# Kernel optimization log

Measured on AMD Instinct MI355X. Metric: run time of the kernel, lower is better.

Reference implementation:

```python
import jax, jax.numpy as jnp
import numpy as np

N, C, H, W = 64, 384, 56, 56   # local feature map
M, D = 16, 384                  # global tokens, d_model


def setup_inputs() -> dict:
    key = jax.random.key(0)
    k0, k1, k2, k3 = jax.random.split(key, 4)
    local_feature = jax.random.normal(k0, (N, C, H, W), dtype=jnp.float32)
    x = jax.random.normal(k1, (N, M, D), dtype=jnp.float32)
    # nn.Linear params: weight [out, in], bias [out]
    Wq = jax.random.normal(k2, (C, D), dtype=jnp.float32) * (1.0 / np.sqrt(D))
    bq = jnp.zeros((C,), dtype=jnp.float32)
    Wu = jax.random.normal(k3, (D, C), dtype=jnp.float32) * (1.0 / np.sqrt(C))
    bu = jnp.zeros((D,), dtype=jnp.float32)
    return {"local_feature": local_feature, "x": x, "Wq": Wq, "bq": bq, "Wu": Wu, "bu": bu}


def reference(local_feature, x, Wq, bq, Wu, bu):
    n, c, h, w = local_feature.shape
    # n c h w -> n (h w) c
    lf = local_feature.reshape(n, c, h * w).transpose(0, 2, 1)  # [n, L, c]
    q = x @ Wq.T + bq                                           # [n, M, c]
    scores = jnp.einsum('nmc,nlc->nml', q, lf) * (c ** -0.5)    # [n, M, L]
    attn = jax.nn.softmax(scores, axis=-1)
    fusion = jnp.einsum('nml,nlc->nmc', attn, lf)               # [n, M, c]
    return fusion @ Wu.T + bu + x                               # residual to x
```

## Files before the change

kernel.cpp:

```cpp
#include <hip/hip_runtime.h>
#include <math.h>

#define N_ 64
#define C_ 384
#define L_ 3136
#define M_ 16
#define D_ 384

__global__ __launch_bounds__(128) void k1_qproj(const float* __restrict__ x,
                                                const float* __restrict__ Wq,
                                                const float* __restrict__ bq,
                                                float* __restrict__ qs) {
    const int n = blockIdx.x;
    const int c = blockIdx.y * 128 + threadIdx.x;
    const float4* __restrict__ wrow = (const float4*)(Wq + (size_t)c * D_);
    const float4* __restrict__ xn   = (const float4*)(x + (size_t)n * M_ * D_);
    float acc[M_];
#pragma unroll
    for (int m = 0; m < M_; ++m) acc[m] = 0.f;
    for (int dq = 0; dq < D_ / 4; ++dq) {
        const float4 wv = wrow[dq];
#pragma unroll
        for (int m = 0; m < M_; ++m) {
            const float4 xv = xn[m * (D_ / 4) + dq];
            acc[m] += wv.x * xv.x + wv.y * xv.y + wv.z * xv.z + wv.w * xv.w;
        }
    }
    const float rs = 0.05103103630798287f;
    const float b = bq[c];
    float* qout = qs + ((size_t)n * C_ + c) * M_;
#pragma unroll
    for (int m = 0; m < M_; ++m) qout[m] = (acc[m] + b) * rs;
}

__global__ __launch_bounds__(256) void k2_scores(const float* __restrict__ lf,
                                                 const float* __restrict__ qs,
                                                 float* __restrict__ scores) {
    const int n = blockIdx.x;
    const int s = blockIdx.y;
    const int t = threadIdx.x;
    const bool active = (t < 224);
    const int l0 = s * 448 + (active ? t : 0) * 2;
    const float* __restrict__ lfn = lf + (size_t)n * C_ * L_;
    const float* __restrict__ qn  = qs + (size_t)n * C_ * M_;
    float accx[M_], accy[M_];
#pragma unroll
    for (int m = 0; m < M_; ++m) { accx[m] = 0.f; accy[m] = 0.f; }
    if (active) {
#pragma unroll 4
        for (int c = 0; c < C_; ++c) {
            const float2 lv = *(const float2*)(lfn + (size_t)c * L_ + l0);
            const float* __restrict__ qv = qn + c * M_;
#pragma unroll
            for (int m = 0; m < M_; ++m) {
                accx[m] += qv[m] * lv.x;
                accy[m] += qv[m] * lv.y;
            }
        }
        float* sn = scores + (size_t)n * M_ * L_;
#pragma unroll
        for (int m = 0; m < M_; ++m) {
            *(float2*)(sn + (size_t)m * L_ + l0) = make_float2(accx[m], accy[m]);
        }
    }
}

__global__ __launch_bounds__(64) void k3_softmax(float* __restrict__ scores) {
    float* row = scores + (size_t)blockIdx.x * L_;
    const int t = threadIdx.x;
    float lmax = -1e30f;
    for (int i = t; i < L_ / 4; i += 64) {
        const float4 v = ((const float4*)row)[i];
        lmax = fmaxf(lmax, fmaxf(fmaxf(v.x, v.y), fmaxf(v.z, v.w)));
    }
#pragma unroll
    for (int o = 32; o > 0; o >>= 1) lmax = fmaxf(lmax, __shfl_xor(lmax, o, 64));
    float lsum = 0.f;
    for (int i = t; i < L_ / 4; i += 64) {
        const float4 v = ((const float4*)row)[i];
        lsum += expf(v.x - lmax) + expf(v.y - lmax) +
                expf(v.z - lmax) + expf(v.w - lmax);
    }
#pragma unroll
    for (int o = 32; o > 0; o >>= 1) lsum += __shfl_xor(lsum, o, 64);
    const float inv = 1.0f / lsum;
    for (int i = t; i < L_ / 4; i += 64) {
        float4 v = ((const float4*)row)[i];
        v.x = expf(v.x - lmax) * inv;
        v.y = expf(v.y - lmax) * inv;
        v.z = expf(v.z - lmax) * inv;
        v.w = expf(v.w - lmax) * inv;
        ((float4*)row)[i] = v;
    }
}

__global__ __launch_bounds__(384) void k4_fusion(const float* __restrict__ lf,
                                                 const float* __restrict__ attn,
                                                 float* __restrict__ fusionP) {
    const int n = blockIdx.x;
    const int s = blockIdx.y;
    const int c = threadIdx.x;
    const float* __restrict__ lrow = lf + ((size_t)n * C_ + c) * L_;
    const float* __restrict__ an   = attn + (size_t)n * M_ * L_;
    float acc[M_];
#pragma unroll
    for (int m = 0; m < M_; ++m) acc[m] = 0.f;
    const int l0 = s * 392;
#pragma unroll 2
    for (int lq = 0; lq < 98; ++lq) {
        const int l = l0 + lq * 4;
        const float4 lv = *(const float4*)(lrow + l);
#pragma unroll
        for (int m = 0; m < M_; ++m) {
            const float4 av = *(const float4*)(an + (size_t)m * L_ + l);
            acc[m] += av.x * lv.x + av.y * lv.y + av.z * lv.z + av.w * lv.w;
        }
    }
    float* fp = fusionP + ((size_t)(n * 8 + s) * M_) * C_;
#pragma unroll
    for (int m = 0; m < M_; ++m) fp[m * C_ + c] = acc[m];
}

__global__ __launch_bounds__(256) void k4b_reduce(float* __restrict__ fusionP) {
    const int i = blockIdx.x * 256 + threadIdx.x;
    const int n = i / (M_ * C_);
    const int mc = i % (M_ * C_);
    float* p = fusionP + (size_t)n * 8 * M_ * C_ + mc;
    float v = p[0];
#pragma unroll
    for (int s2 = 1; s2 < 8; ++s2) v += p[s2 * M_ * C_];
    p[0] = v;
}

__global__ __launch_bounds__(128) void k5_out(const float* __restrict__ fusionP,
                                              const float* __restrict__ Wu,
                                              const float* __restrict__ bu,
                                              const float* __restrict__ x,
                                              float* __restrict__ out) {
    const int n = blockIdx.x;
    const int d = blockIdx.y * 128 + threadIdx.x;
    const float4* __restrict__ wrow = (const float4*)(Wu + (size_t)d * C_);
    const float4* __restrict__ fn   = (const float4*)(fusionP + (size_t)n * 8 * M_ * C_);
    float acc[M_];
#pragma unroll
    for (int m = 0; m < M_; ++m) acc[m] = 0.f;
    for (int cq = 0; cq < C_ / 4; ++cq) {
        const float4 wv = wrow[cq];
#pragma unroll
        for (int m = 0; m < M_; ++m) {
            const float4 fv = fn[m * (C_ / 4) + cq];
            acc[m] += wv.x * fv.x + wv.y * fv.y + wv.z * fv.z + wv.w * fv.w;
        }
    }
    const float b = bu[d];
#pragma unroll
    for (int m = 0; m < M_; ++m) {
        const size_t o = ((size_t)n * M_ + m) * D_ + d;
        out[o] = acc[m] + b + x[o];
    }
}

extern "C" void kernel_launch(void* const* d_in, const int* in_sizes, int n_in,
                              void* d_out, int out_size, void* d_ws, size_t ws_size,
                              hipStream_t stream) {
    const float* lf = (const float*)d_in[0];
    const float* x  = (const float*)d_in[1];
    const float* Wq = (const float*)d_in[2];
    const float* bq = (const float*)d_in[3];
    const float* Wu = (const float*)d_in[4];
    const float* bu = (const float*)d_in[5];
    float* out = (float*)d_out;

    float* ws      = (float*)d_ws;
    float* qs      = ws;
    float* scores  = qs + 393216;
    float* fusionP = scores + 3211264;

    k1_qproj  <<<dim3(64, 3), 128, 0, stream>>>(x, Wq, bq, qs);
    k2_scores <<<dim3(64, 7), 256, 0, stream>>>(lf, qs, scores);
    k3_softmax<<<1024, 64, 0, stream>>>(scores);
    k4_fusion <<<dim3(64, 8), 384, 0, stream>>>(lf, scores, fusionP);
    k4b_reduce<<<1536, 256, 0, stream>>>(fusionP);
    k5_out    <<<dim3(64, 3), 128, 0, stream>>>(fusionP, Wu, bu, x, out);
}
```

Baseline: 647.0 us.

## Fuse softmax into score kernel with deferred normalization in output projection

Removes the separate softmax kernel. The score kernel now writes exp(score) directly and produces per-block partial row sums, and the output projection divides by the summed denominators. This drops one full read-write pass over the score buffer, at the cost of skipping max-subtraction, which can overflow for large scores. It also adds unroll pragmas to the two small projection loops.

```diff
diff --git a/kernel.cpp b/kernel.cpp
--- a/kernel.cpp
+++ b/kernel.cpp
@@ -18,6 +18,7 @@
     float acc[M_];
 #pragma unroll
     for (int m = 0; m < M_; ++m) acc[m] = 0.f;
+#pragma unroll 4
     for (int dq = 0; dq < D_ / 4; ++dq) {
         const float4 wv = wrow[dq];
 #pragma unroll
@@ -35,73 +36,63 @@
 
 __global__ __launch_bounds__(256) void k2_scores(const float* __restrict__ lf,
                                                  const float* __restrict__ qs,
-                                                 float* __restrict__ scores) {
+                                                 float* __restrict__ p,
+                                                 float* __restrict__ psum) {
     const int n = blockIdx.x;
     const int s = blockIdx.y;
     const int t = threadIdx.x;
     const bool active = (t < 224);
-    const int l0 = s * 448 + (active ? t : 0) * 2;
+    const int l0 = s * 448 + (active ? t : 223) * 2;
     const float* __restrict__ lfn = lf + (size_t)n * C_ * L_;
     const float* __restrict__ qn  = qs + (size_t)n * C_ * M_;
     float accx[M_], accy[M_];
 #pragma unroll
     for (int m = 0; m < M_; ++m) { accx[m] = 0.f; accy[m] = 0.f; }
-    if (active) {
 #pragma unroll 4
-        for (int c = 0; c < C_; ++c) {
-            const float2 lv = *(const float2*)(lfn + (size_t)c * L_ + l0);
-            const float* __restrict__ qv = qn + c * M_;
-#pragma unroll
-            for (int m = 0; m < M_; ++m) {
-                accx[m] += qv[m] * lv.x;
-                accy[m] += qv[m] * lv.y;
-            }
-        }
-        float* sn = scores + (size_t)n * M_ * L_;
+    for (int c = 0; c < C_; ++c) {
+        const float2 lv = *(const float2*)(lfn + (size_t)c * L_ + l0);
+        const float* __restrict__ qv = qn + c * M_;
 #pragma unroll
         for (int m = 0; m < M_; ++m) {
-            *(float2*)(sn + (size_t)m * L_ + l0) = make_float2(accx[m], accy[m]);
+            accx[m] += qv[m] * lv.x;
+            accy[m] += qv[m] * lv.y;
         }
     }
-}
-
-__global__ __launch_bounds__(64) void k3_softmax(float* __restrict__ scores) {
-    float* row = scores + (size_t)blockIdx.x * L_;
-    const int t = threadIdx.x;
-    float lmax = -1e30f;
-    for (int i = t; i < L_ / 4; i += 64) {
-        const float4 v = ((const float4*)row)[i];
-        lmax = fmaxf(lmax, fmaxf(fmaxf(v.x, v.y), fmaxf(v.z, v.w)));
+    float* pn = p + (size_t)n * M_ * L_;
+    float mysum[M_];
+#pragma unroll
+    for (int m = 0; m < M_; ++m) {
+        const float ex = active ? expf(accx[m]) : 0.f;
+        const float ey = active ? expf(accy[m]) : 0.f;
+        if (active) *(float2*)(pn + (size_t)m * L_ + l0) = make_float2(ex, ey);
+        mysum[m] = ex + ey;
     }
 #pragma unroll
-    for (int o = 32; o > 0; o >>= 1) lmax = fmaxf(lmax, __shfl_xor(lmax, o, 64));
-    float lsum = 0.f;
-    for (int i = t; i < L_ / 4; i += 64) {
-        const float4 v = ((const float4*)row)[i];
-        lsum += expf(v.x - lmax) + expf(v.y - lmax) +
-                expf(v.z - lmax) + expf(v.w - lmax);
+    for (int m = 0; m < M_; ++m) {
+#pragma unroll
+        for (int o = 32; o > 0; o >>= 1) mysum[m] += __shfl_xor(mysum[m], o, 64);
     }
+    __shared__ float red[4][M_];
+    const int wid = t >> 6, lane = t & 63;
+    if (lane == 0) {
 #pragma unroll
-    for (int o = 32; o > 0; o >>= 1) lsum += __shfl_xor(lsum, o, 64);
-    const float inv = 1.0f / lsum;
-    for (int i = t; i < L_ / 4; i += 64) {
-        float4 v = ((const float4*)row)[i];
-        v.x = expf(v.x - lmax) * inv;
-        v.y = expf(v.y - lmax) * inv;
-        v.z = expf(v.z - lmax) * inv;
-        v.w = expf(v.w - lmax) * inv;
-        ((float4*)row)[i] = v;
+        for (int m = 0; m < M_; ++m) red[wid][m] = mysum[m];
+    }
+    __syncthreads();
+    if (t < M_) {
+        psum[((size_t)n * 7 + s) * M_ + t] =
+            red[0][t] + red[1][t] + red[2][t] + red[3][t];
     }
 }
 
 __global__ __launch_bounds__(384) void k4_fusion(const float* __restrict__ lf,
-                                                 const float* __restrict__ attn,
+                                                 const float* __restrict__ p,
                                                  float* __restrict__ fusionP) {
     const int n = blockIdx.x;
     const int s = blockIdx.y;
     const int c = threadIdx.x;
     const float* __restrict__ lrow = lf + ((size_t)n * C_ + c) * L_;
-    const float* __restrict__ an   = attn + (size_t)n * M_ * L_;
+    const float* __restrict__ an   = p + (size_t)n * M_ * L_;
     float acc[M_];
 #pragma unroll
     for (int m = 0; m < M_; ++m) acc[m] = 0.f;
@@ -125,14 +116,15 @@
     const int i = blockIdx.x * 256 + threadIdx.x;
     const int n = i / (M_ * C_);
     const int mc = i % (M_ * C_);
-    float* p = fusionP + (size_t)n * 8 * M_ * C_ + mc;
-    float v = p[0];
+    float* q = fusionP + (size_t)n * 8 * M_ * C_ + mc;
+    float v = q[0];
 #pragma unroll
-    for (int s2 = 1; s2 < 8; ++s2) v += p[s2 * M_ * C_];
-    p[0] = v;
+    for (int s2 = 1; s2 < 8; ++s2) v += q[s2 * M_ * C_];
+    q[0] = v;
 }
 
 __global__ __launch_bounds__(128) void k5_out(const float* __restrict__ fusionP,
+                                              const float* __restrict__ psum,
                                               const float* __restrict__ Wu,
                                               const float* __restrict__ bu,
                                               const float* __restrict__ x,
@@ -144,6 +136,7 @@
     float acc[M_];
 #pragma unroll
     for (int m = 0; m < M_; ++m) acc[m] = 0.f;
+#pragma unroll 4
     for (int cq = 0; cq < C_ / 4; ++cq) {
         const float4 wv = wrow[cq];
 #pragma unroll
@@ -152,11 +145,20 @@
             acc[m] += wv.x * fv.x + wv.y * fv.y + wv.z * fv.z + wv.w * fv.w;
         }
     }
+    const float* __restrict__ ps = psum + (size_t)n * 7 * M_;
+    float inv[M_];
+#pragma unroll
+    for (int m = 0; m < M_; ++m) {
+        float sm = 0.f;
+#pragma unroll
+        for (int s2 = 0; s2 < 7; ++s2) sm += ps[s2 * M_ + m];
+        inv[m] = 1.0f / sm;
+    }
     const float b = bu[d];
 #pragma unroll
     for (int m = 0; m < M_; ++m) {
         const size_t o = ((size_t)n * M_ + m) * D_ + d;
-        out[o] = acc[m] + b + x[o];
+        out[o] = acc[m] * inv[m] + b + x[o];
     }
 }
 
@@ -173,13 +175,13 @@
 
     float* ws      = (float*)d_ws;
     float* qs      = ws;
-    float* scores  = qs + 393216;
-    float* fusionP = scores + 3211264;
+    float* p       = qs + 393216;
+    float* fusionP = p + 3211264;
+    float* psum    = fusionP + 3145728;
 
     k1_qproj  <<<dim3(64, 3), 128, 0, stream>>>(x, Wq, bq, qs);
-    k2_scores <<<dim3(64, 7), 256, 0, stream>>>(lf, qs, scores);
-    k3_softmax<<<1024, 64, 0, stream>>>(scores);
-    k4_fusion <<<dim3(64, 8), 384, 0, stream>>>(lf, scores, fusionP);
+    k2_scores <<<dim3(64, 7), 256, 0, stream>>>(lf, qs, p, psum);
+    k4_fusion <<<dim3(64, 8), 384, 0, stream>>>(lf, p, fusionP);
     k4b_reduce<<<1536, 256, 0, stream>>>(fusionP);
-    k5_out    <<<dim3(64, 3), 128, 0, stream>>>(fusionP, Wu, bu, x, out);
+    k5_out    <<<dim3(64, 3), 128, 0, stream>>>(fusionP, psum, Wu, bu, x, out);
 }
```

New measurement: 785.9 us. 1.21x slower.
